# Kernel optimization log

Measured on AMD Instinct MI355X. Metric: run time of the kernel, lower is better.

## Reference

```python
import jax, jax.numpy as jnp
import numpy as np
from jax import lax

B, T, I, H = 4096, 64, 8, 128


def _lstm_layer(xs, W_ih, W_hh, b):
    # xs: [T, B, D_in]; PyTorch gate order i, f, g, o
    def step(carry, x_t):
        h, c = carry
        gates = x_t @ W_ih.T + h @ W_hh.T + b  # [B, 4H]
        i, f, g, o = jnp.split(gates, 4, axis=-1)
        i = jax.nn.sigmoid(i)
        f = jax.nn.sigmoid(f)
        g = jnp.tanh(g)
        o = jax.nn.sigmoid(o)
        c_new = f * c + i * g
        h_new = o * jnp.tanh(c_new)
        return (h_new, c_new), h_new

    n_b = xs.shape[1]
    h0 = jnp.zeros((n_b, W_hh.shape[1]), xs.dtype)
    c0 = jnp.zeros((n_b, W_hh.shape[1]), xs.dtype)
    (h_last, _), ys = lax.scan(step, (h0, c0), xs)
    return ys, h_last


def setup_inputs() -> dict:
    key = jax.random.key(0)
    ks = jax.random.split(key, 14)
    s = 1.0 / np.sqrt(H)
    u = lambda k, shape: jax.random.uniform(k, shape, jnp.float32, -s, s)
    return {
        "x": jax.random.normal(ks[0], (B, T, I), jnp.float32),
        "W_ih0": u(ks[1], (4 * H, I)),
        "W_hh0": u(ks[2], (4 * H, H)),
        "b_ih0": u(ks[3], (4 * H,)),
        "b_hh0": u(ks[4], (4 * H,)),
        "W_ih1": u(ks[5], (4 * H, H)),
        "W_hh1": u(ks[6], (4 * H, H)),
        "b_ih1": u(ks[7], (4 * H,)),
        "b_hh1": u(ks[8], (4 * H,)),
        "W_d1": u(ks[9], (5, H)),
        "b_d1": u(ks[10], (5,)),
        "W_d2": u(ks[11], (1, 5)),
        "b_d2": u(ks[12], (1,)),
    }


def reference(x, W_ih0, W_hh0, b_ih0, b_hh0, W_ih1, W_hh1, b_ih1, b_hh1,
              W_d1, b_d1, W_d2, b_d2):
    xs = jnp.transpose(x, (1, 0, 2))  # [T, B, I]
    ys0, _ = _lstm_layer(xs, W_ih0, W_hh0, b_ih0 + b_hh0)
    # inter-layer dropout (p=0.2) and trailing Dropout are identity in eval mode
    _, h_last = _lstm_layer(ys0, W_ih1, W_hh1, b_ih1 + b_hh1)  # [B, H]
    out = jax.nn.relu(h_last)
    out = jax.nn.relu(out @ W_d1.T + b_d1)  # [B, 5]
    out = out @ W_d2.T + b_d2  # [B, 1]
    return out
```

## Files before the change

### kernel.cpp

```cpp
#include <hip/hip_runtime.h>

typedef _Float16 h8 __attribute__((ext_vector_type(8)));
typedef float f4 __attribute__((ext_vector_type(4)));

#define B_ 4096
#define T_ 64
#define I_ 8
#define H_ 128

#define WC0_OFF 0
#define H0_OFF  131072
#define H1_OFF  139264
#define LDS_TOTAL 147456

__device__ __forceinline__ float sigm_(float v) {
    return __builtin_amdgcn_rcpf(1.f + exp2f(-1.4426950408889634f * v));
}
__device__ __forceinline__ float tanh_(float v) {
    return 1.f - 2.f * __builtin_amdgcn_rcpf(exp2f(2.8853900817779268f * v) + 1.f);
}

__global__ __launch_bounds__(512, 2) void lstm_fused_kernel(
    const float* __restrict__ x,
    const float* __restrict__ Wih0, const float* __restrict__ Whh0,
    const float* __restrict__ bih0, const float* __restrict__ bhh0,
    const float* __restrict__ Wih1, const float* __restrict__ Whh1,
    const float* __restrict__ bih1, const float* __restrict__ bhh1,
    const float* __restrict__ Wd1, const float* __restrict__ bd1,
    const float* __restrict__ Wd2, const float* __restrict__ bd2,
    float* __restrict__ out)
{
    __shared__ __align__(16) unsigned char lds[LDS_TOTAL];
    const int tid = threadIdx.x;
    const int w   = tid >> 6;
    const int l   = tid & 63;
    const int c16 = l & 15;
    const int G4  = l >> 4;
    const int rowbase = blockIdx.x * 16;
    const int swzl = (l & 7) << 4;

    {
        const int g  = tid;
        const int gs = (g & 3) * H_ + (g >> 2);
        const float* src = Whh0 + (size_t)gs * H_;
        const int swz = (g & 7) << 4;
        unsigned char* dst = lds + WC0_OFF + g * 256;
#pragma unroll
        for (int kb = 0; kb < 16; kb++) {
            float4 f0 = *(const float4*)(src + kb * 8);
            float4 f1 = *(const float4*)(src + kb * 8 + 4);
            h8 v;
            v[0]=(_Float16)f0.x; v[1]=(_Float16)f0.y; v[2]=(_Float16)f0.z; v[3]=(_Float16)f0.w;
            v[4]=(_Float16)f1.x; v[5]=(_Float16)f1.y; v[6]=(_Float16)f1.z; v[7]=(_Float16)f1.w;
            *(h8*)(dst + ((kb * 16) ^ swz)) = v;
        }
    }
    {
        f4 z = {0.f, 0.f, 0.f, 0.f};
        if (tid < 256) *(f4*)(lds + H0_OFF + 4096 + tid * 16) = z;
        else           *(f4*)(lds + H1_OFF + 4096 + (tid - 256) * 16) = z;
    }

    h8 wc1[4][8];
    h8 ax[4];
    f4 b1[4];
#pragma unroll
    for (int j = 0; j < 4; j++) {
        const int gate = w * 64 + j * 16 + c16;
        const int gs = (gate & 3) * H_ + (gate >> 2);
#pragma unroll
        for (int ks = 0; ks < 8; ks++) {
            const int k0 = ks * 32 + G4 * 8;
            const float* src = (k0 < 128) ? (Whh1 + (size_t)gs * H_ + k0)
                                          : (Wih1 + (size_t)gs * H_ + (k0 - 128));
            float4 f0 = *(const float4*)src;
            float4 f1 = *(const float4*)(src + 4);
            h8 v;
            v[0]=(_Float16)f0.x; v[1]=(_Float16)f0.y; v[2]=(_Float16)f0.z; v[3]=(_Float16)f0.w;
            v[4]=(_Float16)f1.x; v[5]=(_Float16)f1.y; v[6]=(_Float16)f1.z; v[7]=(_Float16)f1.w;
            wc1[j][ks] = v;
        }
        h8 a;
#pragma unroll
        for (int e = 0; e < 8; e++) a[e] = (_Float16)0.f;
        if (G4 == 0) {
            float4 f0 = *(const float4*)(Wih0 + (size_t)gs * I_);
            float4 f1 = *(const float4*)(Wih0 + (size_t)gs * I_ + 4);
            a[0]=(_Float16)f0.x; a[1]=(_Float16)f0.y; a[2]=(_Float16)f0.z; a[3]=(_Float16)f0.w;
            a[4]=(_Float16)f1.x; a[5]=(_Float16)f1.y; a[6]=(_Float16)f1.z; a[7]=(_Float16)f1.w;
        } else if (G4 == 1) {
            a[0] = (_Float16)(bih0[gs] + bhh0[gs]);
        }
        ax[j] = a;
        f4 bb;
#pragma unroll
        for (int q = 0; q < 4; q++) {
            const int gate2 = w * 64 + j * 16 + G4 * 4 + q;
            const int gs2 = (gate2 & 3) * H_ + (gate2 >> 2);
            bb[q] = bih1[gs2] + bhh1[gs2];
        }
        b1[j] = bb;
    }

    const float* xrow = x + (size_t)(rowbase + c16) * T_ * I_;
    float4 xf0 = *(const float4*)(xrow);
    float4 xf1 = *(const float4*)(xrow + 4);

    float c0r[4] = {0.f, 0.f, 0.f, 0.f};
    float c1r[4] = {0.f, 0.f, 0.f, 0.f};

    __syncthreads();

    int cur = 0;
    for (int t = 0; t < T_; t++) {
        h8 bx;
#pragma unroll
        for (int e = 0; e < 8; e++) bx[e] = (_Float16)0.f;
        if (G4 == 0) {
            bx[0]=(_Float16)xf0.x; bx[1]=(_Float16)xf0.y; bx[2]=(_Float16)xf0.z; bx[3]=(_Float16)xf0.w;
            bx[4]=(_Float16)xf1.x; bx[5]=(_Float16)xf1.y; bx[6]=(_Float16)xf1.z; bx[7]=(_Float16)xf1.w;
        } else if (G4 == 1) {
            bx[0] = (_Float16)1.f;
        }
        if (t < T_ - 1) {
            xf0 = *(const float4*)(xrow + (t + 1) * 8);
            xf1 = *(const float4*)(xrow + (t + 1) * 8 + 4);
        }

        f4 acc[4];
        {
            f4 z = {0.f, 0.f, 0.f, 0.f};
#pragma unroll
            for (int j = 0; j < 4; j++) acc[j] = z;
        }
        const unsigned char* h0rd = lds + H0_OFF + (cur ^ 1) * 4096;
#pragma unroll
        for (int ks = 0; ks < 4; ks++) {
            h8 b = *(const h8*)(h0rd + ((c16 * 256 + ks * 64 + G4 * 16) ^ swzl));
#pragma unroll
            for (int j = 0; j < 4; j++) {
                h8 a = *(const h8*)(lds + WC0_OFF + (w * 64 + j * 16 + c16) * 256
                                    + ((ks * 64 + G4 * 16) ^ swzl));
                acc[j] = __builtin_amdgcn_mfma_f32_16x16x32_f16(a, b, acc[j], 0, 0, 0);
            }
        }
#pragma unroll
        for (int j = 0; j < 4; j++)
            acc[j] = __builtin_amdgcn_mfma_f32_16x16x32_f16(ax[j], bx, acc[j], 0, 0, 0);

        unsigned char* h0wr = lds + H0_OFF + cur * 4096;
#pragma unroll
        for (int j = 0; j < 4; j++) {
            const float vi = sigm_(acc[j][0]);
            const float vf = sigm_(acc[j][1]);
            const float vg = tanh_(acc[j][2]);
            const float vo = sigm_(acc[j][3]);
            const float cn = vf * c0r[j] + vi * vg;
            c0r[j] = cn;
            const float hn = vo * tanh_(cn);
            const int u = w * 16 + j * 4 + G4;
            *(_Float16*)(h0wr + ((c16 * 256 + u * 2) ^ swzl)) = (_Float16)hn;
        }

        __syncthreads();

        const unsigned char* h1rd = lds + H1_OFF + (cur ^ 1) * 4096;
        const unsigned char* h0n  = lds + H0_OFF + cur * 4096;
#pragma unroll
        for (int j = 0; j < 4; j++) acc[j] = b1[j];
#pragma unroll
        for (int ks = 0; ks < 4; ks++) {
            h8 b = *(const h8*)(h1rd + ((c16 * 256 + ks * 64 + G4 * 16) ^ swzl));
#pragma unroll
            for (int j = 0; j < 4; j++)
                acc[j] = __builtin_amdgcn_mfma_f32_16x16x32_f16(wc1[j][ks], b, acc[j], 0, 0, 0);
        }
#pragma unroll
        for (int ks = 0; ks < 4; ks++) {
            h8 b = *(const h8*)(h0n + ((c16 * 256 + ks * 64 + G4 * 16) ^ swzl));
#pragma unroll
            for (int j = 0; j < 4; j++)
                acc[j] = __builtin_amdgcn_mfma_f32_16x16x32_f16(wc1[j][ks + 4], b, acc[j], 0, 0, 0);
        }
        unsigned char* h1wr = lds + H1_OFF + cur * 4096;
#pragma unroll
        for (int j = 0; j < 4; j++) {
            const float vi = sigm_(acc[j][0]);
            const float vf = sigm_(acc[j][1]);
            const float vg = tanh_(acc[j][2]);
            const float vo = sigm_(acc[j][3]);
            const float cn = vf * c1r[j] + vi * vg;
            c1r[j] = cn;
            const float hn = vo * tanh_(cn);
            const int u = w * 16 + j * 4 + G4;
            *(_Float16*)(h1wr + ((c16 * 256 + u * 2) ^ swzl)) = (_Float16)hn;
        }
        cur ^= 1;
    }

    __syncthreads();

    if (tid < 128) {
        const int r = tid >> 3, part = tid & 7;
        const unsigned char* h1f = lds + H1_OFF + 4096;
        const int rswz = (r & 7) << 4;
        float s0 = 0.f, s1 = 0.f, s2 = 0.f, s3 = 0.f, s4 = 0.f;
#pragma unroll
        for (int kk = 0; kk < 16; kk++) {
            const int k = part * 16 + kk;
            float a = (float)*(const _Float16*)(h1f + ((r * 256 + k * 2) ^ rswz));
            a = fmaxf(a, 0.f);
            s0 += a * Wd1[0 * H_ + k];
            s1 += a * Wd1[1 * H_ + k];
            s2 += a * Wd1[2 * H_ + k];
            s3 += a * Wd1[3 * H_ + k];
            s4 += a * Wd1[4 * H_ + k];
        }
#pragma unroll
        for (int m = 1; m < 8; m <<= 1) {
            s0 += __shfl_xor(s0, m);
            s1 += __shfl_xor(s1, m);
            s2 += __shfl_xor(s2, m);
            s3 += __shfl_xor(s3, m);
            s4 += __shfl_xor(s4, m);
        }
        if (part == 0) {
            float o = bd2[0];
            o += fmaxf(s0 + bd1[0], 0.f) * Wd2[0];
            o += fmaxf(s1 + bd1[1], 0.f) * Wd2[1];
            o += fmaxf(s2 + bd1[2], 0.f) * Wd2[2];
            o += fmaxf(s3 + bd1[3], 0.f) * Wd2[3];
            o += fmaxf(s4 + bd1[4], 0.f) * Wd2[4];
            out[rowbase + r] = o;
        }
    }
}

extern "C" void kernel_launch(void* const* d_in, const int* in_sizes, int n_in,
                              void* d_out, int out_size, void* d_ws, size_t ws_size,
                              hipStream_t stream)
{
    const float* x    = (const float*)d_in[0];
    const float* Wih0 = (const float*)d_in[1];
    const float* Whh0 = (const float*)d_in[2];
    const float* bih0 = (const float*)d_in[3];
    const float* bhh0 = (const float*)d_in[4];
    const float* Wih1 = (const float*)d_in[5];
    const float* Whh1 = (const float*)d_in[6];
    const float* bih1 = (const float*)d_in[7];
    const float* bhh1 = (const float*)d_in[8];
    const float* Wd1  = (const float*)d_in[9];
    const float* bd1  = (const float*)d_in[10];
    const float* Wd2  = (const float*)d_in[11];
    const float* bd2  = (const float*)d_in[12];

    lstm_fused_kernel<<<B_ / 16, 512, 0, stream>>>(
        x, Wih0, Whh0, bih0, bhh0, Wih1, Whh1, bih1, bhh1,
        Wd1, bd1, Wd2, bd2, (float*)d_out);
}
```

Baseline: 202.2 us.

## Prescale gate weights by log2e and vectorize hidden-state stores

Folds the log2(e) and 2*log2(e) activation scale factors into the fp16 weights and biases at load time, which removes one multiply per gate activation in the recurrent loop. It also permutes the gate-to-row mapping so each lane owns four consecutive hidden units and writes them with one 8-byte LDS store instead of four 2-byte stores. The input/bias MFMA drops from the 16x16x32 to the 16x16x16 variant with a smaller operand. Scaling before the fp16 conversion slightly changes rounding of the weights.

```diff
diff --git a/kernel.cpp b/kernel.cpp
--- a/kernel.cpp
+++ b/kernel.cpp
@@ -1,6 +1,7 @@
 #include <hip/hip_runtime.h>
 
 typedef _Float16 h8 __attribute__((ext_vector_type(8)));
+typedef _Float16 h4 __attribute__((ext_vector_type(4)));
 typedef float f4 __attribute__((ext_vector_type(4)));
 
 #define B_ 4096
@@ -13,11 +14,17 @@
 #define H1_OFF  139264
 #define LDS_TOTAL 147456
 
-__device__ __forceinline__ float sigm_(float v) {
-    return __builtin_amdgcn_rcpf(1.f + exp2f(-1.4426950408889634f * v));
-}
-__device__ __forceinline__ float tanh_(float v) {
-    return 1.f - 2.f * __builtin_amdgcn_rcpf(exp2f(2.8853900817779268f * v) + 1.f);
+#define LOG2E    1.4426950408889634f
+#define TWOLOG2E 2.8853900817779268f
+
+__device__ __forceinline__ float sigm2_(float v) {
+    return __builtin_amdgcn_rcpf(1.f + exp2f(-v));
+}
+__device__ __forceinline__ float tanh2_(float v) {
+    return 1.f - 2.f * __builtin_amdgcn_rcpf(exp2f(v) + 1.f);
+}
+__device__ __forceinline__ float tanhn_(float v) {
+    return 1.f - 2.f * __builtin_amdgcn_rcpf(exp2f(TWOLOG2E * v) + 1.f);
 }
 
 __global__ __launch_bounds__(512, 2) void lstm_fused_kernel(
@@ -40,18 +47,22 @@
     const int swzl = (l & 7) << 4;
 
     {
-        const int g  = tid;
-        const int gs = (g & 3) * H_ + (g >> 2);
+        const int p  = tid;
+        const int q  = p & 3;
+        const int gs = q * H_ + (p >> 6) * 16 + ((p >> 2) & 3) * 4 + ((p >> 4) & 3);
+        const float sc = (q == 2) ? TWOLOG2E : LOG2E;
         const float* src = Whh0 + (size_t)gs * H_;
-        const int swz = (g & 7) << 4;
-        unsigned char* dst = lds + WC0_OFF + g * 256;
+        const int swz = (p & 7) << 4;
+        unsigned char* dst = lds + WC0_OFF + p * 256;
 #pragma unroll
         for (int kb = 0; kb < 16; kb++) {
             float4 f0 = *(const float4*)(src + kb * 8);
             float4 f1 = *(const float4*)(src + kb * 8 + 4);
             h8 v;
-            v[0]=(_Float16)f0.x; v[1]=(_Float16)f0.y; v[2]=(_Float16)f0.z; v[3]=(_Float16)f0.w;
-            v[4]=(_Float16)f1.x; v[5]=(_Float16)f1.y; v[6]=(_Float16)f1.z; v[7]=(_Float16)f1.w;
+            v[0]=(_Float16)(f0.x*sc); v[1]=(_Float16)(f0.y*sc);
+            v[2]=(_Float16)(f0.z*sc); v[3]=(_Float16)(f0.w*sc);
+            v[4]=(_Float16)(f1.x*sc); v[5]=(_Float16)(f1.y*sc);
+            v[6]=(_Float16)(f1.z*sc); v[7]=(_Float16)(f1.w*sc);
             *(h8*)(dst + ((kb * 16) ^ swz)) = v;
         }
     }
@@ -62,44 +73,46 @@
     }
 
     h8 wc1[4][8];
-    h8 ax[4];
+    h4 ax16[4];
     f4 b1[4];
-#pragma unroll
-    for (int j = 0; j < 4; j++) {
-        const int gate = w * 64 + j * 16 + c16;
-        const int gs = (gate & 3) * H_ + (gate >> 2);
-#pragma unroll
-        for (int ks = 0; ks < 8; ks++) {
-            const int k0 = ks * 32 + G4 * 8;
-            const float* src = (k0 < 128) ? (Whh1 + (size_t)gs * H_ + k0)
-                                          : (Wih1 + (size_t)gs * H_ + (k0 - 128));
-            float4 f0 = *(const float4*)src;
-            float4 f1 = *(const float4*)(src + 4);
-            h8 v;
-            v[0]=(_Float16)f0.x; v[1]=(_Float16)f0.y; v[2]=(_Float16)f0.z; v[3]=(_Float16)f0.w;
-            v[4]=(_Float16)f1.x; v[5]=(_Float16)f1.y; v[6]=(_Float16)f1.z; v[7]=(_Float16)f1.w;
-            wc1[j][ks] = v;
-        }
-        h8 a;
-#pragma unroll
-        for (int e = 0; e < 8; e++) a[e] = (_Float16)0.f;
-        if (G4 == 0) {
-            float4 f0 = *(const float4*)(Wih0 + (size_t)gs * I_);
-            float4 f1 = *(const float4*)(Wih0 + (size_t)gs * I_ + 4);
-            a[0]=(_Float16)f0.x; a[1]=(_Float16)f0.y; a[2]=(_Float16)f0.z; a[3]=(_Float16)f0.w;
-            a[4]=(_Float16)f1.x; a[5]=(_Float16)f1.y; a[6]=(_Float16)f1.z; a[7]=(_Float16)f1.w;
-        } else if (G4 == 1) {
-            a[0] = (_Float16)(bih0[gs] + bhh0[gs]);
-        }
-        ax[j] = a;
-        f4 bb;
-#pragma unroll
-        for (int q = 0; q < 4; q++) {
-            const int gate2 = w * 64 + j * 16 + G4 * 4 + q;
-            const int gs2 = (gate2 & 3) * H_ + (gate2 >> 2);
-            bb[q] = bih1[gs2] + bhh1[gs2];
-        }
-        b1[j] = bb;
+    {
+        const int rq = c16 & 3;
+        const float sc1 = (rq == 2) ? TWOLOG2E : LOG2E;
+#pragma unroll
+        for (int j = 0; j < 4; j++) {
+            const int gs = rq * H_ + w * 16 + (c16 >> 2) * 4 + j;
+#pragma unroll
+            for (int ks = 0; ks < 8; ks++) {
+                const int k0 = ks * 32 + G4 * 8;
+                const float* src = (k0 < 128) ? (Whh1 + (size_t)gs * H_ + k0)
+                                              : (Wih1 + (size_t)gs * H_ + (k0 - 128));
+                float4 f0 = *(const float4*)src;
+                float4 f1 = *(const float4*)(src + 4);
+                h8 v;
+                v[0]=(_Float16)(f0.x*sc1); v[1]=(_Float16)(f0.y*sc1);
+                v[2]=(_Float16)(f0.z*sc1); v[3]=(_Float16)(f0.w*sc1);
+                v[4]=(_Float16)(f1.x*sc1); v[5]=(_Float16)(f1.y*sc1);
+                v[6]=(_Float16)(f1.z*sc1); v[7]=(_Float16)(f1.w*sc1);
+                wc1[j][ks] = v;
+            }
+            h4 a;
+#pragma unroll
+            for (int e = 0; e < 4; e++) {
+                const int k = G4 * 4 + e;
+                float val = 0.f;
+                if (k < 8)       val = Wih0[(size_t)gs * I_ + k] * sc1;
+                else if (k == 8) val = (bih0[gs] + bhh0[gs]) * sc1;
+                a[e] = (_Float16)val;
+            }
+            ax16[j] = a;
+            f4 bb;
+#pragma unroll
+            for (int q2 = 0; q2 < 4; q2++) {
+                const int gs2 = q2 * H_ + w * 16 + G4 * 4 + j;
+                bb[q2] = (bih1[gs2] + bhh1[gs2]) * ((q2 == 2) ? TWOLOG2E : LOG2E);
+            }
+            b1[j] = bb;
+        }
     }
 
     const float* xrow = x + (size_t)(rowbase + c16) * T_ * I_;
@@ -113,13 +126,16 @@
 
     int cur = 0;
     for (int t = 0; t < T_; t++) {
-        h8 bx;
-#pragma unroll
-        for (int e = 0; e < 8; e++) bx[e] = (_Float16)0.f;
+        h4 bx;
+        bx[0] = (_Float16)0.f; bx[1] = (_Float16)0.f;
+        bx[2] = (_Float16)0.f; bx[3] = (_Float16)0.f;
         if (G4 == 0) {
-            bx[0]=(_Float16)xf0.x; bx[1]=(_Float16)xf0.y; bx[2]=(_Float16)xf0.z; bx[3]=(_Float16)xf0.w;
-            bx[4]=(_Float16)xf1.x; bx[5]=(_Float16)xf1.y; bx[6]=(_Float16)xf1.z; bx[7]=(_Float16)xf1.w;
+            bx[0]=(_Float16)xf0.x; bx[1]=(_Float16)xf0.y;
+            bx[2]=(_Float16)xf0.z; bx[3]=(_Float16)xf0.w;
         } else if (G4 == 1) {
+            bx[0]=(_Float16)xf1.x; bx[1]=(_Float16)xf1.y;
+            bx[2]=(_Float16)xf1.z; bx[3]=(_Float16)xf1.w;
+        } else if (G4 == 2) {
             bx[0] = (_Float16)1.f;
         }
         if (t < T_ - 1) {
@@ -146,20 +162,22 @@
         }
 #pragma unroll
         for (int j = 0; j < 4; j++)
-            acc[j] = __builtin_amdgcn_mfma_f32_16x16x32_f16(ax[j], bx, acc[j], 0, 0, 0);
+            acc[j] = __builtin_amdgcn_mfma_f32_16x16x16f16(ax16[j], bx, acc[j], 0, 0, 0);
 
         unsigned char* h0wr = lds + H0_OFF + cur * 4096;
-#pragma unroll
-        for (int j = 0; j < 4; j++) {
-            const float vi = sigm_(acc[j][0]);
-            const float vf = sigm_(acc[j][1]);
-            const float vg = tanh_(acc[j][2]);
-            const float vo = sigm_(acc[j][3]);
-            const float cn = vf * c0r[j] + vi * vg;
-            c0r[j] = cn;
-            const float hn = vo * tanh_(cn);
-            const int u = w * 16 + j * 4 + G4;
-            *(_Float16*)(h0wr + ((c16 * 256 + u * 2) ^ swzl)) = (_Float16)hn;
+        {
+            h4 hv;
+#pragma unroll
+            for (int j = 0; j < 4; j++) {
+                const float vi = sigm2_(acc[j][0]);
+                const float vf = sigm2_(acc[j][1]);
+                const float vg = tanh2_(acc[j][2]);
+                const float vo = sigm2_(acc[j][3]);
+                const float cn = vf * c0r[j] + vi * vg;
+                c0r[j] = cn;
+                hv[j] = (_Float16)(vo * tanhn_(cn));
+            }
+            *(h4*)(h0wr + ((c16 * 256 + w * 32 + G4 * 8) ^ swzl)) = hv;
         }
 
         __syncthreads();
@@ -183,17 +201,19 @@
                 acc[j] = __builtin_amdgcn_mfma_f32_16x16x32_f16(wc1[j][ks + 4], b, acc[j], 0, 0, 0);
         }
         unsigned char* h1wr = lds + H1_OFF + cur * 4096;
-#pragma unroll
-        for (int j = 0; j < 4; j++) {
-            const float vi = sigm_(acc[j][0]);
-            const float vf = sigm_(acc[j][1]);
-            const float vg = tanh_(acc[j][2]);
-            const float vo = sigm_(acc[j][3]);
-            const float cn = vf * c1r[j] + vi * vg;
-            c1r[j] = cn;
-            const float hn = vo * tanh_(cn);
-            const int u = w * 16 + j * 4 + G4;
-            *(_Float16*)(h1wr + ((c16 * 256 + u * 2) ^ swzl)) = (_Float16)hn;
+        {
+            h4 hv;
+#pragma unroll
+            for (int j = 0; j < 4; j++) {
+                const float vi = sigm2_(acc[j][0]);
+                const float vf = sigm2_(acc[j][1]);
+                const float vg = tanh2_(acc[j][2]);
+                const float vo = sigm2_(acc[j][3]);
+                const float cn = vf * c1r[j] + vi * vg;
+                c1r[j] = cn;
+                hv[j] = (_Float16)(vo * tanhn_(cn));
+            }
+            *(h4*)(h1wr + ((c16 * 256 + w * 32 + G4 * 8) ^ swzl)) = hv;
         }
         cur ^= 1;
     }
```

Result: no change. 202.0 us (-0.1%).
